# Optimization experiments

Hardware: AMD Instinct MI355X
Metric: run time of the kernel (lower is better)

Reference implementation:

```python
import jax, jax.numpy as jnp
import numpy as np

H, NH, HD = 1024, 16, 64
WIN = 256
W = WIN // 2  # one-sided window
EXP = 4
PAD_VAL = 0.0  # pad_token_id
B, S0 = 2, 2048
NEG = float(np.finfo(np.float32).min)


def setup_inputs() -> dict:
    key = jax.random.key(0)
    ks = jax.random.split(key, 12)

    def lin(k, fi, fo):
        k1, k2 = jax.random.split(k)
        w = jax.random.normal(k1, (fi, fo), jnp.float32) / np.float32(np.sqrt(fi))
        b = jax.random.normal(k2, (fo,), jnp.float32) * 0.02
        return w, b

    x = jax.random.normal(ks[0], (B, S0, H), jnp.float32)
    mask = jnp.zeros((B, S0), jnp.int32)  # 0 = real token, 1 = pad
    wq, bq = lin(ks[1], H, H)
    wk, bk = lin(ks[2], H, H)
    wv, bv = lin(ks[3], H, H)
    wqg, bqg = lin(ks[4], H, H)
    wkg, bkg = lin(ks[5], H, H)
    wvg, bvg = lin(ks[6], H, H)
    ln_g = jnp.ones((H,), jnp.float32)
    ln_b = jnp.zeros((H,), jnp.float32)
    w1, b1 = lin(ks[7], H, H * EXP)
    w2, b2 = lin(ks[8], H * EXP, H)
    return dict(x=x, mask=mask, wq=wq, bq=bq, wk=wk, bk=bk, wv=wv, bv=bv,
                wqg=wqg, bqg=bqg, wkg=wkg, bkg=bkg, wvg=wvg, bvg=bvg,
                ln_g=ln_g, ln_b=ln_b, w1=w1, b1=b1, w2=w2, b2=b2)


def _forward(x, mask, wq, bq, wk, bk, wv, bv, wqg, bqg, wkg, bkg, wvg, bvg,
             ln_g, ln_b, w1, b1, w2, b2):
    Bsz, s0, _ = x.shape
    pad = WIN - s0 % WIN
    xp = jnp.pad(x, ((0, 0), (0, pad), (0, 0)), constant_values=PAD_VAL)
    m = jnp.pad(mask, ((0, 0), (0, pad)), constant_values=1)
    S = s0 + pad
    lm = (m * -10000).at[:, -1].set(10000)  # [B,S]; task='cls': last token global
    is_masked = lm < 0
    remove = lm != 0  # masked OR global keys removed from local windows

    inv_sqrt = np.float32(1.0 / np.sqrt(HD))
    q = ((xp @ wq + bq) * inv_sqrt).reshape(Bsz, S, NH, HD)
    k = (xp @ wk + bk).reshape(Bsz, S, NH, HD)
    v = (xp @ wv + bv).reshape(Bsz, S, NH, HD)

    nc = S // W
    # chunked banded scores: query chunk of W attends to 3W keys (prev/self/next)
    qc = q.transpose(0, 2, 1, 3).reshape(Bsz, NH, nc, W, HD)
    kpad = jnp.pad(k.transpose(0, 2, 1, 3), ((0, 0), (0, 0), (W, W), (0, 0)))
    idx3w = jnp.arange(nc)[:, None] * W + jnp.arange(3 * W)[None, :]  # [nc,3W]
    kc = kpad[:, :, idx3w]  # [B,NH,nc,3W,HD]
    sc = jnp.einsum('bhcpd,bhckd->bhcpk', qc, kc)  # [B,NH,nc,W,3W]
    p_idx = jnp.arange(W)[:, None]
    d_idx = jnp.arange(2 * W + 1)[None, :]
    band = sc[:, :, :, p_idx, p_idx + d_idx]  # [B,NH,nc,W,2W+1]
    band = band.reshape(Bsz, NH, S, 2 * W + 1).transpose(0, 2, 1, 3)  # [B,S,NH,2W+1]

    # key index j = i + d - W for offset d in [0, 2W]
    j = jnp.arange(S)[:, None] + jnp.arange(2 * W + 1)[None, :] - W
    in_range = (j >= 0) & (j < S)
    jc = jnp.clip(j, 0, S - 1)
    fmask = jnp.where(remove, NEG, 0.0)  # [B,S]
    band = band + fmask[:, jc][:, :, None, :]
    band = jnp.where(in_range[None, :, None, :], band, -jnp.inf)

    # global key column (single global token = last position), concatenated in front
    gcol = jnp.einsum('bshd,bhd->bsh', q, k[:, -1])[..., None]  # [B,S,NH,1]
    scores = jnp.concatenate([gcol, band], axis=-1)  # [B,S,NH,2W+2]
    probs = jax.nn.softmax(scores, axis=-1)
    probs = jnp.where(is_masked[:, :, None, None], 0.0, probs)

    out_g = probs[..., 0][..., None] * v[:, -1][:, None]  # [B,S,NH,HD]
    lp = probs[..., 1:].transpose(0, 2, 1, 3).reshape(Bsz, NH, nc, W, 2 * W + 1)
    pc = jnp.zeros((Bsz, NH, nc, W, 3 * W), probs.dtype).at[:, :, :, p_idx, p_idx + d_idx].set(lp)
    vpad = jnp.pad(v.transpose(0, 2, 1, 3), ((0, 0), (0, 0), (W, W), (0, 0)))
    vc = vpad[:, :, idx3w]  # [B,NH,nc,3W,HD]
    out_l = jnp.einsum('bhcpk,bhckd->bhcpd', pc, vc).reshape(Bsz, NH, S, HD).transpose(0, 2, 1, 3)
    attn = (out_l + out_g).reshape(Bsz, S, H)

    # full global attention for the global token (separate projections)
    qg = ((xp[:, -1] @ wqg + bqg) * inv_sqrt).reshape(Bsz, NH, HD)
    kg = (xp @ wkg + bkg).reshape(Bsz, S, NH, HD)
    vg = (xp @ wvg + bvg).reshape(Bsz, S, NH, HD)
    gs = jnp.einsum('bhd,bshd->bhs', qg, kg)
    gs = jnp.where(is_masked[:, None, :], NEG, gs)
    gout = jnp.einsum('bhs,bshd->bhd', jax.nn.softmax(gs, axis=-1), vg).reshape(Bsz, H)
    attn = attn.at[:, -1].set(gout)

    y = (xp + attn)[:, :s0]  # residual then strip padding
    mu = y.mean(-1, keepdims=True)
    var = ((y - mu) ** 2).mean(-1, keepdims=True)
    y = (y - mu) * jax.lax.rsqrt(var + 1e-5) * ln_g + ln_b
    h = jax.nn.gelu(y @ w1 + b1, approximate=False)
    return y + (h @ w2 + b2)


def reference(x, mask, wq, bq, wk, bk, wv, bv, wqg, bqg, wkg, bkg, wvg, bvg,
              ln_g, ln_b, w1, b1, w2, b2):
    return _forward(x, mask, wq, bq, wk, bk, wv, bv, wqg, bqg, wkg, bkg,
                    wvg, bvg, ln_g, ln_b, w1, b1, w2, b2)
```

## Files before the change

### kernel.cpp

```cpp
#include <hip/hip_runtime.h>


using bf16x8 = __attribute__((ext_vector_type(8))) short;
using bf16x4 = __attribute__((ext_vector_type(4))) short;
using f32x4  = __attribute__((ext_vector_type(4))) float;

__device__ __forceinline__ float b2f(short s) {
    return __uint_as_float(((unsigned int)(unsigned short)s) << 16);
}
__device__ __forceinline__ short f2b(float f) {
    unsigned int u = __float_as_uint(f);
    u += 0x7fffu + ((u >> 16) & 1u);
    return (short)(u >> 16);
}
__device__ __forceinline__ f32x4 mfma16(bf16x8 a, bf16x8 b, f32x4 c) {
    return __builtin_amdgcn_mfma_f32_16x16x32_bf16(a, b, c, 0, 0, 0);
}
__device__ __forceinline__ float safe_exp(float x) {
    return expf((x <= 0.f) ? x : 0.f);
}
__device__ __forceinline__ float fast_gelu(float v) {
    float z  = fabsf(v) * 0.70710678118f;
    float t  = __builtin_amdgcn_rcpf(fmaf(0.47047f, z, 1.f));
    float e  = __expf(-z * z);
    float p  = t * fmaf(t, fmaf(t, 0.7478556f, -0.0958798f), 0.3480242f);
    float er = fmaf(-p, e, 1.f);
    er = (v < 0.f) ? -er : er;
    return 0.5f * v * (1.f + er);
}
__device__ __forceinline__ void load_lds16(const short* g, short* l) {
    __builtin_amdgcn_global_load_lds((const __attribute__((address_space(1))) void*)g,
                                     (__attribute__((address_space(3))) void*)l, 16, 0, 0);
}
__device__ __forceinline__ int xcd_swizzle_flat() {
    int fid = blockIdx.x + blockIdx.y * gridDim.x;
    int nwg = gridDim.x * gridDim.y;
    return (fid & 7) * (nwg >> 3) + (fid >> 3);
}
#define NEGF (-3.0e38f)

__global__ void cvt_f32_bf16(const float* __restrict__ in, short* __restrict__ out, int n) {
    int i = (blockIdx.x * 256 + threadIdx.x) * 4;
    f32x4 v = *(const f32x4*)(in + i);
    bf16x4 o;
#pragma unroll
    for (int j = 0; j < 4; ++j) o[j] = f2b(v[j]);
    *(bf16x4*)(out + i) = o;
}

__global__ void cvt_transpose(const float* __restrict__ in, short* __restrict__ out,
                              int R, int C) {
    __shared__ short tile[32][33];
    int bx = blockIdx.x * 32, by = blockIdx.y * 32;
    int tx = threadIdx.x, ty = threadIdx.y;
    for (int i = ty; i < 32; i += 8)
        tile[i][tx] = f2b(in[(size_t)(by + i) * C + bx + tx]);
    __syncthreads();
    for (int i = ty; i < 32; i += 8)
        out[(size_t)(bx + i) * R + by + tx] = tile[tx][i];
}

__global__ void cvt_transpose_qkv(const float* __restrict__ wq, const float* __restrict__ wk,
                                  const float* __restrict__ wv, short* __restrict__ out) {
    __shared__ short tile[32][33];
    const float* in = (blockIdx.z == 0) ? wq : (blockIdx.z == 1) ? wk : wv;
    short* dst = out + (size_t)blockIdx.z * 1024 * 1024;
    int bx = blockIdx.x * 32, by = blockIdx.y * 32;
    int tx = threadIdx.x, ty = threadIdx.y;
    for (int i = ty; i < 32; i += 8)
        tile[i][tx] = f2b(in[(size_t)(by + i) * 1024 + bx + tx]);
    __syncthreads();
    for (int i = ty; i < 32; i += 8)
        dst[(size_t)(bx + i) * 1024 + by + tx] = tile[tx][i];
}

__global__ __launch_bounds__(256, 4) void gemm_bt(
    const short* __restrict__ A, const short* __restrict__ Bt,
    const float* __restrict__ bias0, const float* __restrict__ bias1,
    const float* __restrict__ bias2,
    short* __restrict__ C, short* __restrict__ Vt,
    int M, int N, int K, float scale, int mode)
{
    __shared__ short sh[128 * 136];
    short* As = sh;
    short* Bs = sh + 8192;
    int swz = xcd_swizzle_flat();
    int m0 = (swz % gridDim.x) * 128, n0 = (swz / gridDim.x) * 128;
    int t = threadIdx.x;
    int wave = t >> 6, lane = t & 63, quad = lane >> 4, l16 = lane & 15;
    int wr = (wave >> 1) * 64, wc = (wave & 1) * 64;

    const short* ap[4]; const short* bp[4]; short* la[4]; short* lb[4];
    int gk = (((lane & 7) ^ (lane >> 3)) * 8);
#pragma unroll
    for (int l = 0; l < 4; ++l) {
        int c = wave * 4 + l;
        int row = c * 8 + (lane >> 3);
        ap[l] = A  + (size_t)(m0 + row) * K + gk;
        bp[l] = Bt + (size_t)(n0 + row) * K + gk;
        la[l] = As + c * 512;
        lb[l] = Bs + c * 512;
    }
    int sw = l16 & 7;

    f32x4 acc[4][4] = {};
    for (int k0 = 0; k0 < K; k0 += 64) {
#pragma unroll
        for (int l = 0; l < 4; ++l) { load_lds16(ap[l] + k0, la[l]); load_lds16(bp[l] + k0, lb[l]); }
        __syncthreads();
#pragma unroll
        for (int ks = 0; ks < 2; ++ks) {
            int slot = ((ks * 4 + quad) ^ sw) * 8;
            bf16x8 af[4], bfr[4];
#pragma unroll
            for (int i = 0; i < 4; ++i)
                af[i] = *(bf16x8*)(As + (wr + i * 16 + l16) * 64 + slot);
#pragma unroll
            for (int j = 0; j < 4; ++j)
                bfr[j] = *(bf16x8*)(Bs + (wc + j * 16 + l16) * 64 + slot);
#pragma unroll
            for (int i = 0; i < 4; ++i)
#pragma unroll
                for (int j = 0; j < 4; ++j)
                    acc[i][j] = mfma16(af[i], bfr[j], acc[i][j]);
        }
        __syncthreads();
    }

    int seg0 = n0 >> 10;
    if (mode == 1 || seg0 < 2) {
        if (mode == 1) {
#pragma unroll
            for (int j = 0; j < 4; ++j) {
                int col = n0 + wc + j * 16 + l16;
                float bs = bias0[col];
#pragma unroll
                for (int i = 0; i < 4; ++i)
#pragma unroll
                    for (int r = 0; r < 4; ++r) {
                        float v = fast_gelu(acc[i][j][r] + bs);
                        sh[(wr + i * 16 + quad * 4 + r) * 136 + wc + j * 16 + l16] = f2b(v);
                    }
            }
        } else {
            float sc = (seg0 == 0) ? scale : 1.0f;
            const float* bpt = (seg0 == 0) ? bias0 : bias1;
#pragma unroll
            for (int j = 0; j < 4; ++j) {
                int col = n0 + wc + j * 16 + l16;
                float bs = bpt[col & 1023];
#pragma unroll
                for (int i = 0; i < 4; ++i)
#pragma unroll
                    for (int r = 0; r < 4; ++r)
                        sh[(wr + i * 16 + quad * 4 + r) * 136 + wc + j * 16 + l16] =
                            f2b((acc[i][j][r] + bs) * sc);
            }
        }
        __syncthreads();
        int row = t >> 1, half = t & 1;
        const short* src = sh + row * 136 + half * 64;
        short* dst = C + (size_t)(m0 + row) * N + n0 + half * 64;
#pragma unroll
        for (int cgk = 0; cgk < 8; ++cgk)
            *(bf16x8*)(dst + cgk * 8) = *(const bf16x8*)(src + cgk * 8);
    } else {
#pragma unroll
        for (int j = 0; j < 4; ++j) {
            int cl = wc + j * 16 + l16;
            float bs = bias2[(n0 & 1023) + cl];
#pragma unroll
            for (int i = 0; i < 4; ++i)
#pragma unroll
                for (int r = 0; r < 4; ++r)
                    sh[cl * 136 + wr + i * 16 + quad * 4 + r] = f2b(acc[i][j][r] + bs);
        }
        __syncthreads();
        int h0 = (n0 & 1023) >> 6;
        int bb = m0 >> 11, s0 = m0 & 2047;
        int sc = t & 15;
#pragma unroll
        for (int cgk = 0; cgk < 8; ++cgk) {
            int cl = (t >> 4) + cgk * 16;
            int h = h0 + (cl >> 6), d = cl & 63;
            *(bf16x8*)(Vt + (((size_t)(bb * 16 + h)) * 64 + d) * 2048 + s0 + sc * 8) =
                *(const bf16x8*)(sh + cl * 136 + sc * 8);
        }
    }
}

__global__ __launch_bounds__(256, 4) void gemm64_db(
    const short* __restrict__ A, const short* __restrict__ Bt,
    const float* __restrict__ bias, const float* __restrict__ resf,
    float* __restrict__ Cf, int M, int N, int K)
{
    __shared__ short As[2][64 * 64];
    __shared__ short Bs[2][64 * 64];
    int m0 = blockIdx.x * 64, n0 = blockIdx.y * 64;
    int t = threadIdx.x;
    int wave = t >> 6, lane = t & 63, quad = lane >> 4, l16 = lane & 15;
    int wr = (wave >> 1) * 32, wc = (wave & 1) * 32;

    const short* ap[2]; const short* bp[2]; int lo[2];
    int gk = (((lane & 7) ^ (lane >> 3)) * 8);
#pragma unroll
    for (int l = 0; l < 2; ++l) {
        int c = wave * 2 + l;
        int row = c * 8 + (lane >> 3);
        ap[l] = A  + (size_t)(m0 + row) * K + gk;
        bp[l] = Bt + (size_t)(n0 + row) * K + gk;
        lo[l] = c * 512;
    }
    int sw = l16 & 7;

    const int nt = K >> 6;
#pragma unroll
    for (int l = 0; l < 2; ++l) { load_lds16(ap[l], &As[0][lo[l]]); load_lds16(bp[l], &Bs[0][lo[l]]); }

    f32x4 acc[2][2] = {};
    for (int ti = 0; ti < nt; ++ti) {
        int cur = ti & 1;
        if (ti + 1 < nt) {
            int k0 = (ti + 1) << 6;
#pragma unroll
            for (int l = 0; l < 2; ++l) {
                load_lds16(ap[l] + k0, &As[cur ^ 1][lo[l]]);
                load_lds16(bp[l] + k0, &Bs[cur ^ 1][lo[l]]);
            }
            asm volatile("s_waitcnt vmcnt(4)" ::: "memory");
        } else {
            asm volatile("s_waitcnt vmcnt(0)" ::: "memory");
        }
        __builtin_amdgcn_s_barrier();
        asm volatile("" ::: "memory");

        const short* as = &As[cur][0];
        const short* bs = &Bs[cur][0];
#pragma unroll
        for (int ks = 0; ks < 2; ++ks) {
            int slot = ((ks * 4 + quad) ^ sw) * 8;
            bf16x8 af[2], bfr[2];
#pragma unroll
            for (int i = 0; i < 2; ++i)
                af[i] = *(bf16x8*)(as + (wr + i * 16 + l16) * 64 + slot);
#pragma unroll
            for (int j = 0; j < 2; ++j)
                bfr[j] = *(bf16x8*)(bs + (wc + j * 16 + l16) * 64 + slot);
#pragma unroll
            for (int i = 0; i < 2; ++i)
#pragma unroll
                for (int j = 0; j < 2; ++j)
                    acc[i][j] = mfma16(af[i], bfr[j], acc[i][j]);
        }
        asm volatile("" ::: "memory");
        __builtin_amdgcn_s_barrier();
    }

#pragma unroll
    for (int j = 0; j < 2; ++j) {
        int col = n0 + wc + j * 16 + l16;
        float bs = bias[col];
#pragma unroll
        for (int i = 0; i < 2; ++i) {
#pragma unroll
            for (int r = 0; r < 4; ++r) {
                int row = m0 + wr + i * 16 + quad * 4 + r;
                Cf[(size_t)row * N + col] = acc[i][j][r] + bs + resf[(size_t)row * N + col];
            }
        }
    }
}

__global__ __launch_bounds__(256, 2) void attn_kernel(
    const short* __restrict__ QKV, const short* __restrict__ Vt,
    const int* __restrict__ mask,
    const float* __restrict__ bk, const float* __restrict__ bv,
    short* __restrict__ attn)
{
    extern __shared__ char smem[];
    short* PsQ = (short*)smem;
    short* KV  = (short*)(smem + 34816);
    float* gkf = (float*)(smem + 53248);
    float* gvf = (float*)(smem + 53504);

    int blk = blockIdx.x;
    int c = blk & 15, h = (blk >> 4) & 15, b = blk >> 8;
    int t = threadIdx.x;
    int wave = t >> 6, lane = t & 63, quad = lane >> 4, l16 = lane & 15;
    int q0 = c * 128;
    const int bs_off = b * 2048;
    const short* Q = QKV + h * 64;
    const short* K = QKV + 1024 + h * 64;

#pragma unroll
    for (int l = 0; l < 4; ++l) {
        int idx = l * 256 + t;
        int p = idx >> 3, dc = (idx & 7) * 8;
        *(bf16x8*)(PsQ + p * 72 + dc) =
            *(const bf16x8*)(Q + ((size_t)(bs_off + q0 + p)) * 3072 + dc);
    }
    if (t < 64) { gkf[t] = bk[h * 64 + t]; gvf[t] = bv[h * 64 + t]; }
    __syncthreads();

    bf16x8 aq[2][2];
#pragma unroll
    for (int ti = 0; ti < 2; ++ti)
#pragma unroll
        for (int ks = 0; ks < 2; ++ks)
            aq[ti][ks] = *(bf16x8*)(PsQ + (wave * 32 + ti * 16 + l16) * 72 + ks * 32 + quad * 8);

    float s_g[2][4];
#pragma unroll
    for (int ti = 0; ti < 2; ++ti)
#pragma unroll
        for (int r = 0; r < 4; ++r) {
            int row = wave * 32 + ti * 16 + quad * 4 + r;
            float part = 0.f;
#pragma unroll
            for (int dd = 0; dd < 4; ++dd) {
                int d = l16 * 4 + dd;
                part += b2f(PsQ[row * 72 + d]) * gkf[d];
            }
#pragma unroll
            for (int dsh = 1; dsh < 16; dsh <<= 1) part += __shfl_xor(part, dsh);
            s_g[ti][r] = part;
        }

    f32x4 o_acc[2][4] = {};
    float m_run[2][4], l_run[2][4];
#pragma unroll
    for (int ti = 0; ti < 2; ++ti)
#pragma unroll
        for (int r = 0; r < 4; ++r) { m_run[ti][r] = NEGF; l_run[ti][r] = 0.f; }

    int kt_beg = (q0 == 0) ? 1 : 0;
    int kt_end = (q0 + 256 > 2048) ? 2 : 3;
    for (int kt = kt_beg; kt < kt_end; ++kt) {
        int jb = q0 + (kt - 1) * 128;
        __syncthreads();
#pragma unroll
        for (int l = 0; l < 4; ++l) {
            int idx = l * 256 + t;
            int p = idx >> 3, dc = (idx & 7) * 8;
            *(bf16x8*)(KV + p * 72 + dc) =
                *(const bf16x8*)(K + ((size_t)(bs_off + jb + p)) * 3072 + dc);
        }
        __syncthreads();

        f32x4 s_acc[2][8] = {};
#pragma unroll
        for (int ks = 0; ks < 2; ++ks) {
            bf16x8 bk8[8];
#pragma unroll
            for (int tj = 0; tj < 8; ++tj)
                bk8[tj] = *(bf16x8*)(KV + (tj * 16 + l16) * 72 + ks * 32 + quad * 8);
#pragma unroll
            for (int ti = 0; ti < 2; ++ti)
#pragma unroll
                for (int tj = 0; tj < 8; ++tj)
                    s_acc[ti][tj] = mfma16(aq[ti][ks], bk8[tj], s_acc[ti][tj]);
        }

        float negj[8]; int jcol[8];
#pragma unroll
        for (int tj = 0; tj < 8; ++tj) {
            jcol[tj] = jb + tj * 16 + l16;
            negj[tj] = (mask[bs_off + jcol[tj]] != 0) ? NEGF : 0.f;
        }
        float tmax[2][4];
#pragma unroll
        for (int ti = 0; ti < 2; ++ti)
#pragma unroll
            for (int r = 0; r < 4; ++r) tmax[ti][r] = NEGF;
#pragma unroll
        for (int ti = 0; ti < 2; ++ti) {
            int irow_base = q0 + wave * 32 + ti * 16 + quad * 4;
#pragma unroll
            for (int tj = 0; tj < 8; ++tj)
#pragma unroll
                for (int r = 0; r < 4; ++r) {
                    int dj = jcol[tj] - (irow_base + r);
                    float sc = (dj >= -128 && dj <= 128) ? (s_acc[ti][tj][r] + negj[tj]) : NEGF;
                    s_acc[ti][tj][r] = sc;
                    tmax[ti][r] = fmaxf(tmax[ti][r], sc);
                }
        }
#pragma unroll
        for (int ti = 0; ti < 2; ++ti)
#pragma unroll
            for (int r = 0; r < 4; ++r)
#pragma unroll
                for (int dsh = 1; dsh < 16; dsh <<= 1)
                    tmax[ti][r] = fmaxf(tmax[ti][r], __shfl_xor(tmax[ti][r], dsh));

        float alpha[2][4], lsum[2][4];
#pragma unroll
        for (int ti = 0; ti < 2; ++ti)
#pragma unroll
            for (int r = 0; r < 4; ++r) {
                float mnew = fmaxf(m_run[ti][r], tmax[ti][r]);
                alpha[ti][r] = safe_exp(m_run[ti][r] - mnew);
                m_run[ti][r] = mnew;
                lsum[ti][r] = 0.f;
            }
#pragma unroll
        for (int ti = 0; ti < 2; ++ti)
#pragma unroll
            for (int tj = 0; tj < 8; ++tj)
#pragma unroll
                for (int r = 0; r < 4; ++r) {
                    float p = safe_exp(s_acc[ti][tj][r] - m_run[ti][r]);
                    lsum[ti][r] += p;
                    PsQ[(wave * 32 + ti * 16 + quad * 4 + r) * 136 + tj * 16 + l16] = f2b(p);
                }
#pragma unroll
        for (int ti = 0; ti < 2; ++ti)
#pragma unroll
            for (int r = 0; r < 4; ++r) {
#pragma unroll
                for (int dsh = 1; dsh < 16; dsh <<= 1) lsum[ti][r] += __shfl_xor(lsum[ti][r], dsh);
                l_run[ti][r] = l_run[ti][r] * alpha[ti][r] + lsum[ti][r];
            }
#pragma unroll
        for (int ti = 0; ti < 2; ++ti)
#pragma unroll
            for (int dj = 0; dj < 4; ++dj)
#pragma unroll
                for (int r = 0; r < 4; ++r) o_acc[ti][dj][r] *= alpha[ti][r];

        __syncthreads();
#pragma unroll
        for (int l = 0; l < 4; ++l) {
            int idx = l * 256 + t;
            int d = idx >> 4, kc = (idx & 15) * 8;
            *(bf16x8*)(KV + d * 136 + kc) =
                *(const bf16x8*)(Vt + ((size_t)(b * 16 + h) * 64 + d) * 2048 + jb + kc);
        }
        __syncthreads();
#pragma unroll
        for (int ks = 0; ks < 4; ++ks) {
            bf16x8 ap[2], bv8[4];
#pragma unroll
            for (int ti = 0; ti < 2; ++ti)
                ap[ti] = *(bf16x8*)(PsQ + (wave * 32 + ti * 16 + l16) * 136 + ks * 32 + quad * 8);
#pragma unroll
            for (int dj = 0; dj < 4; ++dj)
                bv8[dj] = *(bf16x8*)(KV + (dj * 16 + l16) * 136 + ks * 32 + quad * 8);
#pragma unroll
            for (int ti = 0; ti < 2; ++ti)
#pragma unroll
                for (int dj = 0; dj < 4; ++dj)
                    o_acc[ti][dj] = mfma16(ap[ti], bv8[dj], o_acc[ti][dj]);
        }
    }

#pragma unroll
    for (int ti = 0; ti < 2; ++ti) {
        int irow_base = q0 + wave * 32 + ti * 16 + quad * 4;
#pragma unroll
        for (int r = 0; r < 4; ++r) {
            int i = irow_base + r;
            float m2 = fmaxf(m_run[ti][r], s_g[ti][r]);
            float pg = safe_exp(s_g[ti][r] - m2);
            float al = safe_exp(m_run[ti][r] - m2);
            float l2 = l_run[ti][r] * al + pg;
            float invl = 1.f / fmaxf(l2, 1e-30f);
            float qm = (mask[bs_off + i] > 0) ? 0.f : 1.f;
#pragma unroll
            for (int dj = 0; dj < 4; ++dj) {
                int d = dj * 16 + l16;
                float val = (o_acc[ti][dj][r] * al + pg * gvf[d]) * invl * qm;
                attn[((size_t)(bs_off + i)) * 1024 + h * 64 + d] = f2b(val);
            }
        }
    }
}

__global__ __launch_bounds__(256) void resid_ln(
    const float* __restrict__ x, const short* __restrict__ attn,
    const float* __restrict__ g, const float* __restrict__ be,
    short* __restrict__ yb, float* __restrict__ yf)
{
    int row = blockIdx.x, t = threadIdx.x;
    int lane = t & 63, wave = t >> 6;
    const size_t base = (size_t)row * 1024;
    float v[4]; float s = 0.f, s2 = 0.f;
#pragma unroll
    for (int i = 0; i < 4; ++i) {
        int c = i * 256 + t;
        float val = x[base + c] + b2f(attn[base + c]);
        v[i] = val; s += val; s2 += val * val;
    }
#pragma unroll
    for (int off = 32; off > 0; off >>= 1) { s += __shfl_xor(s, off); s2 += __shfl_xor(s2, off); }
    __shared__ float red[8];
    if (lane == 0) { red[wave] = s; red[4 + wave] = s2; }
    __syncthreads();
    s  = red[0] + red[1] + red[2] + red[3];
    s2 = red[4] + red[5] + red[6] + red[7];
    float mu  = s * (1.f / 1024.f);
    float var = s2 * (1.f / 1024.f) - mu * mu;
    float inv = rsqrtf(fmaxf(var, 0.f) + 1e-5f);
#pragma unroll
    for (int i = 0; i < 4; ++i) {
        int c = i * 256 + t;
        float o = (v[i] - mu) * inv * g[c] + be[c];
        yb[base + c] = f2b(o);
        yf[base + c] = o;
    }
}

static constexpr size_t MEG      = 1048576;
static constexpr size_t OFF_WQKV = 0;
static constexpr size_t OFF_W1T  = 3 * MEG;
static constexpr size_t OFF_W2T  = 7 * MEG;
static constexpr size_t OFF_XB   = 11 * MEG;
static constexpr size_t OFF_QKV  = 15 * MEG;
static constexpr size_t OFF_VT   = 27 * MEG;
static constexpr size_t OFF_ATT  = 31 * MEG;
static constexpr size_t OFF_YN   = 35 * MEG;
static constexpr size_t OFF_YF   = 39 * MEG;
static constexpr size_t OFF_H    = OFF_QKV;

extern "C" void kernel_launch(void* const* d_in, const int* in_sizes, int n_in,
                              void* d_out, int out_size, void* d_ws, size_t ws_size,
                              hipStream_t stream) {
    (void)in_sizes; (void)n_in; (void)out_size; (void)ws_size;
    const float* x    = (const float*)d_in[0];
    const int*   mask = (const int*)  d_in[1];
    const float* wq   = (const float*)d_in[2];
    const float* bq   = (const float*)d_in[3];
    const float* wk   = (const float*)d_in[4];
    const float* bk   = (const float*)d_in[5];
    const float* wv   = (const float*)d_in[6];
    const float* bv   = (const float*)d_in[7];
    const float* lng  = (const float*)d_in[14];
    const float* lnb  = (const float*)d_in[15];
    const float* w1   = (const float*)d_in[16];
    const float* b1   = (const float*)d_in[17];
    const float* w2   = (const float*)d_in[18];
    const float* b2   = (const float*)d_in[19];
    short* ws  = (short*)d_ws;
    float* out = (float*)d_out;

    dim3 tb(32, 8);
    cvt_transpose_qkv<<<dim3(32, 32, 3), tb, 0, stream>>>(wq, wk, wv, ws + OFF_WQKV);
    cvt_transpose<<<dim3(128, 32), tb, 0, stream>>>(w1, ws + OFF_W1T, 1024, 4096);
    cvt_transpose<<<dim3(32, 128), tb, 0, stream>>>(w2, ws + OFF_W2T, 4096, 1024);
    cvt_f32_bf16<<<4096, 256, 0, stream>>>(x, ws + OFF_XB, 4194304);

    gemm_bt<<<dim3(32, 24), 256, 0, stream>>>(ws + OFF_XB, ws + OFF_WQKV,
                                              bq, bk, bv,
                                              ws + OFF_QKV, ws + OFF_VT,
                                              4096, 3072, 1024, 0.125f, 0);

    attn_kernel<<<512, 256, 53760, stream>>>(ws + OFF_QKV, ws + OFF_VT,
                                             mask, bk, bv, ws + OFF_ATT);

    resid_ln<<<4096, 256, 0, stream>>>(x, ws + OFF_ATT, lng, lnb,
                                       ws + OFF_YN, (float*)(ws + OFF_YF));

    gemm_bt<<<dim3(32, 32), 256, 0, stream>>>(ws + OFF_YN, ws + OFF_W1T,
                                              b1, nullptr, nullptr,
                                              ws + OFF_H, nullptr,
                                              4096, 4096, 1024, 1.0f, 1);
    gemm64_db<<<dim3(64, 16), 256, 0, stream>>>(ws + OFF_H, ws + OFF_W2T,
                                                b2, (const float*)(ws + OFF_YF),
                                                out, 4096, 1024, 4096);
}
```

Measured before the change: 339.5 us.

## Halve attention query tile, prefetch K/V into registers, drop GEMM XCD swizzle

The attention kernel now processes 64 query rows per block instead of 128, doubling the grid to 1024 blocks and cutting LDS so four blocks can fit per CU. K and V tiles are prefetched into registers and written to LDS around lighter LDS-only barriers, overlapping global loads with compute, and out-of-range key rows are clamped and masked. The GEMM drops its XCD-aware block swizzle in favour of plain block indexing, and safe_exp switches to the fast __expf. The smaller query tile means K/V are loaded twice as often overall, and removing the swizzle may hurt L2 locality in the GEMMs.

```diff
diff --git a/kernel.cpp b/kernel.cpp
--- a/kernel.cpp
+++ b/kernel.cpp
@@ -17,7 +17,7 @@
     return __builtin_amdgcn_mfma_f32_16x16x32_bf16(a, b, c, 0, 0, 0);
 }
 __device__ __forceinline__ float safe_exp(float x) {
-    return expf((x <= 0.f) ? x : 0.f);
+    return __expf((x <= 0.f) ? x : 0.f);
 }
 __device__ __forceinline__ float fast_gelu(float v) {
     float z  = fabsf(v) * 0.70710678118f;
@@ -32,10 +32,10 @@
     __builtin_amdgcn_global_load_lds((const __attribute__((address_space(1))) void*)g,
                                      (__attribute__((address_space(3))) void*)l, 16, 0, 0);
 }
-__device__ __forceinline__ int xcd_swizzle_flat() {
-    int fid = blockIdx.x + blockIdx.y * gridDim.x;
-    int nwg = gridDim.x * gridDim.y;
-    return (fid & 7) * (nwg >> 3) + (fid >> 3);
+__device__ __forceinline__ void barrier_lds_only() {
+    asm volatile("s_waitcnt lgkmcnt(0)" ::: "memory");
+    __builtin_amdgcn_s_barrier();
+    asm volatile("" ::: "memory");
 }
 #define NEGF (-3.0e38f)
 
@@ -84,8 +84,7 @@
     __shared__ short sh[128 * 136];
     short* As = sh;
     short* Bs = sh + 8192;
-    int swz = xcd_swizzle_flat();
-    int m0 = (swz % gridDim.x) * 128, n0 = (swz / gridDim.x) * 128;
+    int m0 = blockIdx.x * 128, n0 = blockIdx.y * 128;
     int t = threadIdx.x;
     int wave = t >> 6, lane = t & 63, quad = lane >> 4, l16 = lane & 15;
     int wr = (wave >> 1) * 64, wc = (wave & 1) * 64;
@@ -271,7 +270,7 @@
     }
 }
 
-__global__ __launch_bounds__(256, 2) void attn_kernel(
+__global__ __launch_bounds__(256, 4) void attn_kernel(
     const short* __restrict__ QKV, const short* __restrict__ Vt,
     const int* __restrict__ mask,
     const float* __restrict__ bk, const float* __restrict__ bv,
@@ -279,21 +278,22 @@
 {
     extern __shared__ char smem[];
     short* PsQ = (short*)smem;
-    short* KV  = (short*)(smem + 34816);
-    float* gkf = (float*)(smem + 53248);
-    float* gvf = (float*)(smem + 53504);
+    short* KV  = (short*)(smem + 17408);
+    float* gkf = (float*)(smem + 35840);
+    float* gvf = (float*)(smem + 36096);
 
     int blk = blockIdx.x;
-    int c = blk & 15, h = (blk >> 4) & 15, b = blk >> 8;
+    int c = blk & 31, h = (blk >> 5) & 15, b = blk >> 9;
     int t = threadIdx.x;
     int wave = t >> 6, lane = t & 63, quad = lane >> 4, l16 = lane & 15;
-    int q0 = c * 128;
+    int q0 = c * 64;
     const int bs_off = b * 2048;
     const short* Q = QKV + h * 64;
     const short* K = QKV + 1024 + h * 64;
-
-#pragma unroll
-    for (int l = 0; l < 4; ++l) {
+    const short* Vg = Vt + (size_t)(b * 16 + h) * 64 * 2048;
+
+#pragma unroll
+    for (int l = 0; l < 2; ++l) {
         int idx = l * 256 + t;
         int p = idx >> 3, dc = (idx & 7) * 8;
         *(bf16x8*)(PsQ + p * 72 + dc) =
@@ -302,52 +302,63 @@
     if (t < 64) { gkf[t] = bk[h * 64 + t]; gvf[t] = bv[h * 64 + t]; }
     __syncthreads();
 
-    bf16x8 aq[2][2];
-#pragma unroll
-    for (int ti = 0; ti < 2; ++ti)
-#pragma unroll
-        for (int ks = 0; ks < 2; ++ks)
-            aq[ti][ks] = *(bf16x8*)(PsQ + (wave * 32 + ti * 16 + l16) * 72 + ks * 32 + quad * 8);
-
-    float s_g[2][4];
-#pragma unroll
-    for (int ti = 0; ti < 2; ++ti)
-#pragma unroll
-        for (int r = 0; r < 4; ++r) {
-            int row = wave * 32 + ti * 16 + quad * 4 + r;
-            float part = 0.f;
-#pragma unroll
-            for (int dd = 0; dd < 4; ++dd) {
-                int d = l16 * 4 + dd;
-                part += b2f(PsQ[row * 72 + d]) * gkf[d];
-            }
-#pragma unroll
-            for (int dsh = 1; dsh < 16; dsh <<= 1) part += __shfl_xor(part, dsh);
-            s_g[ti][r] = part;
-        }
-
-    f32x4 o_acc[2][4] = {};
-    float m_run[2][4], l_run[2][4];
-#pragma unroll
-    for (int ti = 0; ti < 2; ++ti)
-#pragma unroll
-        for (int r = 0; r < 4; ++r) { m_run[ti][r] = NEGF; l_run[ti][r] = 0.f; }
+    bf16x8 aq[2];
+#pragma unroll
+    for (int ks = 0; ks < 2; ++ks)
+        aq[ks] = *(bf16x8*)(PsQ + (wave * 16 + l16) * 72 + ks * 32 + quad * 8);
+
+    float s_g[4];
+#pragma unroll
+    for (int r = 0; r < 4; ++r) {
+        int row = wave * 16 + quad * 4 + r;
+        float part = 0.f;
+#pragma unroll
+        for (int dd = 0; dd < 4; ++dd) {
+            int d = l16 * 4 + dd;
+            part += b2f(PsQ[row * 72 + d]) * gkf[d];
+        }
+#pragma unroll
+        for (int dsh = 1; dsh < 16; dsh <<= 1) part += __shfl_xor(part, dsh);
+        s_g[r] = part;
+    }
+
+    f32x4 o_acc[4] = {};
+    float m_run[4], l_run[4];
+#pragma unroll
+    for (int r = 0; r < 4; ++r) { m_run[r] = NEGF; l_run[r] = 0.f; }
 
     int kt_beg = (q0 == 0) ? 1 : 0;
-    int kt_end = (q0 + 256 > 2048) ? 2 : 3;
+    int kt_end = (q0 + 128 < 2048) ? 3 : 2;
+
+    bf16x8 kreg[4], vreg[4];
+    {
+        int jb = q0 + (kt_beg - 1) * 128;
+#pragma unroll
+        for (int l = 0; l < 4; ++l) {
+            int idx = l * 256 + t;
+            int row = jb + (idx >> 3);
+            row = (row < 0) ? 0 : ((row > 2047) ? 2047 : row);
+            kreg[l] = *(const bf16x8*)(K + ((size_t)(bs_off + row)) * 3072 + (idx & 7) * 8);
+        }
+    }
+
     for (int kt = kt_beg; kt < kt_end; ++kt) {
         int jb = q0 + (kt - 1) * 128;
-        __syncthreads();
 #pragma unroll
         for (int l = 0; l < 4; ++l) {
             int idx = l * 256 + t;
-            int p = idx >> 3, dc = (idx & 7) * 8;
-            *(bf16x8*)(KV + p * 72 + dc) =
-                *(const bf16x8*)(K + ((size_t)(bs_off + jb + p)) * 3072 + dc);
-        }
-        __syncthreads();
-
-        f32x4 s_acc[2][8] = {};
+            *(bf16x8*)(KV + (idx >> 3) * 72 + (idx & 7) * 8) = kreg[l];
+        }
+#pragma unroll
+        for (int l = 0; l < 4; ++l) {
+            int idx = l * 256 + t;
+            int s0 = jb + (idx & 15) * 8;
+            s0 = (s0 < 0) ? 0 : ((s0 > 2040) ? 2040 : s0);
+            vreg[l] = *(const bf16x8*)(Vg + ((size_t)(idx >> 4)) * 2048 + s0);
+        }
+        barrier_lds_only();
+
+        f32x4 s_acc[8] = {};
 #pragma unroll
         for (int ks = 0; ks < 2; ++ks) {
             bf16x8 bk8[8];
@@ -355,123 +366,112 @@
             for (int tj = 0; tj < 8; ++tj)
                 bk8[tj] = *(bf16x8*)(KV + (tj * 16 + l16) * 72 + ks * 32 + quad * 8);
 #pragma unroll
-            for (int ti = 0; ti < 2; ++ti)
-#pragma unroll
-                for (int tj = 0; tj < 8; ++tj)
-                    s_acc[ti][tj] = mfma16(aq[ti][ks], bk8[tj], s_acc[ti][tj]);
+            for (int tj = 0; tj < 8; ++tj)
+                s_acc[tj] = mfma16(aq[ks], bk8[tj], s_acc[tj]);
         }
 
         float negj[8]; int jcol[8];
 #pragma unroll
         for (int tj = 0; tj < 8; ++tj) {
             jcol[tj] = jb + tj * 16 + l16;
-            negj[tj] = (mask[bs_off + jcol[tj]] != 0) ? NEGF : 0.f;
-        }
-        float tmax[2][4];
-#pragma unroll
-        for (int ti = 0; ti < 2; ++ti)
-#pragma unroll
-            for (int r = 0; r < 4; ++r) tmax[ti][r] = NEGF;
-#pragma unroll
-        for (int ti = 0; ti < 2; ++ti) {
-            int irow_base = q0 + wave * 32 + ti * 16 + quad * 4;
-#pragma unroll
-            for (int tj = 0; tj < 8; ++tj)
-#pragma unroll
-                for (int r = 0; r < 4; ++r) {
-                    int dj = jcol[tj] - (irow_base + r);
-                    float sc = (dj >= -128 && dj <= 128) ? (s_acc[ti][tj][r] + negj[tj]) : NEGF;
-                    s_acc[ti][tj][r] = sc;
-                    tmax[ti][r] = fmaxf(tmax[ti][r], sc);
-                }
-        }
-#pragma unroll
-        for (int ti = 0; ti < 2; ++ti)
-#pragma unroll
-            for (int r = 0; r < 4; ++r)
-#pragma unroll
-                for (int dsh = 1; dsh < 16; dsh <<= 1)
-                    tmax[ti][r] = fmaxf(tmax[ti][r], __shfl_xor(tmax[ti][r], dsh));
-
-        float alpha[2][4], lsum[2][4];
-#pragma unroll
-        for (int ti = 0; ti < 2; ++ti)
+            bool jv = (jcol[tj] >= 0) && (jcol[tj] < 2048);
+            int jc = jv ? jcol[tj] : 0;
+            negj[tj] = (!jv || (mask[bs_off + jc] != 0)) ? NEGF : 0.f;
+        }
+        float tmax[4];
+#pragma unroll
+        for (int r = 0; r < 4; ++r) tmax[r] = NEGF;
+        int irow_base = q0 + wave * 16 + quad * 4;
+#pragma unroll
+        for (int tj = 0; tj < 8; ++tj)
 #pragma unroll
             for (int r = 0; r < 4; ++r) {
-                float mnew = fmaxf(m_run[ti][r], tmax[ti][r]);
-                alpha[ti][r] = safe_exp(m_run[ti][r] - mnew);
-                m_run[ti][r] = mnew;
-                lsum[ti][r] = 0.f;
-            }
-#pragma unroll
-        for (int ti = 0; ti < 2; ++ti)
-#pragma unroll
-            for (int tj = 0; tj < 8; ++tj)
-#pragma unroll
-                for (int r = 0; r < 4; ++r) {
-                    float p = safe_exp(s_acc[ti][tj][r] - m_run[ti][r]);
-                    lsum[ti][r] += p;
-                    PsQ[(wave * 32 + ti * 16 + quad * 4 + r) * 136 + tj * 16 + l16] = f2b(p);
-                }
-#pragma unroll
-        for (int ti = 0; ti < 2; ++ti)
+                int dj = jcol[tj] - (irow_base + r);
+                float sc = (dj >= -128 && dj <= 128) ? (s_acc[tj][r] + negj[tj]) : NEGF;
+                s_acc[tj][r] = sc;
+                tmax[r] = fmaxf(tmax[r], sc);
+            }
+#pragma unroll
+        for (int r = 0; r < 4; ++r)
+#pragma unroll
+            for (int dsh = 1; dsh < 16; dsh <<= 1)
+                tmax[r] = fmaxf(tmax[r], __shfl_xor(tmax[r], dsh));
+
+        float alpha[4], lsum[4];
+#pragma unroll
+        for (int r = 0; r < 4; ++r) {
+            float mnew = fmaxf(m_run[r], tmax[r]);
+            alpha[r] = safe_exp(m_run[r] - mnew);
+            m_run[r] = mnew;
+            lsum[r] = 0.f;
+        }
+#pragma unroll
+        for (int tj = 0; tj < 8; ++tj)
 #pragma unroll
             for (int r = 0; r < 4; ++r) {
-#pragma unroll
-                for (int dsh = 1; dsh < 16; dsh <<= 1) lsum[ti][r] += __shfl_xor(lsum[ti][r], dsh);
-                l_run[ti][r] = l_run[ti][r] * alpha[ti][r] + lsum[ti][r];
-            }
-#pragma unroll
-        for (int ti = 0; ti < 2; ++ti)
-#pragma unroll
-            for (int dj = 0; dj < 4; ++dj)
-#pragma unroll
-                for (int r = 0; r < 4; ++r) o_acc[ti][dj][r] *= alpha[ti][r];
-
-        __syncthreads();
+                float p = safe_exp(s_acc[tj][r] - m_run[r]);
+                lsum[r] += p;
+                PsQ[(wave * 16 + quad * 4 + r) * 136 + tj * 16 + l16] = f2b(p);
+            }
+#pragma unroll
+        for (int r = 0; r < 4; ++r) {
+#pragma unroll
+            for (int dsh = 1; dsh < 16; dsh <<= 1) lsum[r] += __shfl_xor(lsum[r], dsh);
+            l_run[r] = l_run[r] * alpha[r] + lsum[r];
+        }
+#pragma unroll
+        for (int dj = 0; dj < 4; ++dj)
+#pragma unroll
+            for (int r = 0; r < 4; ++r) o_acc[dj][r] *= alpha[r];
+
+        barrier_lds_only();
+
 #pragma unroll
         for (int l = 0; l < 4; ++l) {
             int idx = l * 256 + t;
-            int d = idx >> 4, kc = (idx & 15) * 8;
-            *(bf16x8*)(KV + d * 136 + kc) =
-                *(const bf16x8*)(Vt + ((size_t)(b * 16 + h) * 64 + d) * 2048 + jb + kc);
-        }
-        __syncthreads();
+            *(bf16x8*)(KV + (idx >> 4) * 136 + (idx & 15) * 8) = vreg[l];
+        }
+        if (kt + 1 < kt_end) {
+            int jb2 = q0 + kt * 128;
+#pragma unroll
+            for (int l = 0; l < 4; ++l) {
+                int idx = l * 256 + t;
+                int row = jb2 + (idx >> 3);
+                row = (row < 0) ? 0 : ((row > 2047) ? 2047 : row);
+                kreg[l] = *(const bf16x8*)(K + ((size_t)(bs_off + row)) * 3072 + (idx & 7) * 8);
+            }
+        }
+        barrier_lds_only();
+
 #pragma unroll
         for (int ks = 0; ks < 4; ++ks) {
-            bf16x8 ap[2], bv8[4];
-#pragma unroll
-            for (int ti = 0; ti < 2; ++ti)
-                ap[ti] = *(bf16x8*)(PsQ + (wave * 32 + ti * 16 + l16) * 136 + ks * 32 + quad * 8);
+            bf16x8 ap, bv8[4];
+            ap = *(bf16x8*)(PsQ + (wave * 16 + l16) * 136 + ks * 32 + quad * 8);
 #pragma unroll
             for (int dj = 0; dj < 4; ++dj)
                 bv8[dj] = *(bf16x8*)(KV + (dj * 16 + l16) * 136 + ks * 32 + quad * 8);
 #pragma unroll
-            for (int ti = 0; ti < 2; ++ti)
-#pragma unroll
-                for (int dj = 0; dj < 4; ++dj)
-                    o_acc[ti][dj] = mfma16(ap[ti], bv8[dj], o_acc[ti][dj]);
-        }
-    }
-
-#pragma unroll
-    for (int ti = 0; ti < 2; ++ti) {
-        int irow_base = q0 + wave * 32 + ti * 16 + quad * 4;
-#pragma unroll
-        for (int r = 0; r < 4; ++r) {
-            int i = irow_base + r;
-            float m2 = fmaxf(m_run[ti][r], s_g[ti][r]);
-            float pg = safe_exp(s_g[ti][r] - m2);
-            float al = safe_exp(m_run[ti][r] - m2);
-            float l2 = l_run[ti][r] * al + pg;
-            float invl = 1.f / fmaxf(l2, 1e-30f);
-            float qm = (mask[bs_off + i] > 0) ? 0.f : 1.f;
-#pragma unroll
-            for (int dj = 0; dj < 4; ++dj) {
-                int d = dj * 16 + l16;
-                float val = (o_acc[ti][dj][r] * al + pg * gvf[d]) * invl * qm;
-                attn[((size_t)(bs_off + i)) * 1024 + h * 64 + d] = f2b(val);
-            }
+            for (int dj = 0; dj < 4; ++dj)
+                o_acc[dj] = mfma16(ap, bv8[dj], o_acc[dj]);
+        }
+        barrier_lds_only();
+    }
+
+    int irow_base = q0 + wave * 16 + quad * 4;
+#pragma unroll
+    for (int r = 0; r < 4; ++r) {
+        int i = irow_base + r;
+        float m2 = fmaxf(m_run[r], s_g[r]);
+        float pg = safe_exp(s_g[r] - m2);
+        float al = safe_exp(m_run[r] - m2);
+        float l2 = l_run[r] * al + pg;
+        float invl = 1.f / fmaxf(l2, 1e-30f);
+        float qm = (mask[bs_off + i] > 0) ? 0.f : 1.f;
+#pragma unroll
+        for (int dj = 0; dj < 4; ++dj) {
+            int d = dj * 16 + l16;
+            float val = (o_acc[dj][r] * al + pg * gvf[d]) * invl * qm;
+            attn[((size_t)(bs_off + i)) * 1024 + h * 64 + d] = f2b(val);
         }
     }
 }
@@ -554,8 +554,8 @@
                                               ws + OFF_QKV, ws + OFF_VT,
                                               4096, 3072, 1024, 0.125f, 0);
 
-    attn_kernel<<<512, 256, 53760, stream>>>(ws + OFF_QKV, ws + OFF_VT,
-                                             mask, bk, bv, ws + OFF_ATT);
+    attn_kernel<<<1024, 256, 36352, stream>>>(ws + OFF_QKV, ws + OFF_VT,
+                                              mask, bk, bv, ws + OFF_ATT);
 
     resid_ln<<<4096, 256, 0, stream>>>(x, ws + OFF_ATT, lng, lnb,
                                        ws + OFF_YN, (float*)(ws + OFF_YF));
```

Result: no change. 345.9 us (+1.9%).
